# Kernel tuning notes

Measured on AMD Instinct MI355X. Metric: run time of the kernel, lower is better.

The kernel has to match this reference:

```python
import jax, jax.numpy as jnp
import numpy as np

EMBED = 1024

def setup_inputs() -> dict:
    key = jax.random.key(0)
    ks = jax.random.split(key, 7)
    s = 1.0 / np.sqrt(EMBED)
    x = jax.random.normal(ks[0], (8, 2048, EMBED), dtype=jnp.float32)
    Wq = jax.random.normal(ks[1], (EMBED, EMBED), dtype=jnp.float32) * s
    bq = jax.random.normal(ks[2], (EMBED,), dtype=jnp.float32) * s
    Wk = jax.random.normal(ks[3], (EMBED, EMBED), dtype=jnp.float32) * s
    bk = jax.random.normal(ks[4], (EMBED,), dtype=jnp.float32) * s
    Wv = jax.random.normal(ks[5], (EMBED, EMBED), dtype=jnp.float32) * s
    bv = jax.random.normal(ks[6], (EMBED,), dtype=jnp.float32) * s
    return {"x": x, "Wq": Wq, "bq": bq, "Wk": Wk, "bk": bk, "Wv": Wv, "bv": bv}

def reference(x, Wq, bq, Wk, bk, Wv, bv):
    # Linear layers: y = x @ W^T + b (torch convention)
    Q = jnp.einsum('bse,fe->bsf', x, Wq) + bq
    K = jnp.einsum('bse,fe->bsf', x, Wk) + bk
    V = jnp.einsum('bse,fe->bsf', x, Wv) + bv
    scale = 1.0 / jnp.sqrt(jnp.asarray(x.shape[-1], x.dtype))
    scores = jnp.einsum('bqe,bke->bqk', Q, K) * scale  # [B, S, S]
    weights = jax.nn.softmax(scores, axis=-1)
    # dropout is identity in eval mode (deterministic reference)
    return jnp.einsum('bqk,bke->bqe', weights, V)
```

## Files before the change

kernel.cpp:

```cpp
#include <hip/hip_runtime.h>

typedef __bf16 bf16x8 __attribute__((ext_vector_type(8)));
typedef float f32x4 __attribute__((ext_vector_type(4)));

__device__ __forceinline__ unsigned short f2bf(float f) {
  unsigned int u = __builtin_bit_cast(unsigned int, f);
  u += 0x7fffu + ((u >> 16) & 1u);
  return (unsigned short)(u >> 16);
}

__device__ __forceinline__ void async16(const void* g, void* l) {
  __builtin_amdgcn_global_load_lds(
      (const __attribute__((address_space(1))) unsigned int*)g,
      (__attribute__((address_space(3))) unsigned int*)l, 16, 0, 0);
}

#define MFMA(a, b, c) __builtin_amdgcn_mfma_f32_16x16x32_bf16((a), (b), (c), 0, 0, 0)

__global__ __launch_bounds__(256) void pack_bf16(const float* __restrict__ src,
                                                 unsigned short* __restrict__ dst,
                                                 long n) {
  long i = ((long)blockIdx.x * blockDim.x + threadIdx.x) * 4;
  long stride = (long)gridDim.x * blockDim.x * 4;
  for (; i < n; i += stride) {
    float4 v = *(const float4*)(src + i);
    ushort4 o;
    o.x = f2bf(v.x); o.y = f2bf(v.y); o.z = f2bf(v.z); o.w = f2bf(v.w);
    *(ushort4*)(dst + i) = o;
  }
}

__global__ __launch_bounds__(256) void pack_w3(const float* __restrict__ s0,
                                               const float* __restrict__ s1,
                                               const float* __restrict__ s2,
                                               unsigned short* __restrict__ dst) {
  const float* s = (blockIdx.y == 0) ? s0 : (blockIdx.y == 1) ? s1 : s2;
  long i = ((long)blockIdx.x * 256 + threadIdx.x) * 4;
  float4 v = *(const float4*)(s + i);
  ushort4 o;
  o.x = f2bf(v.x); o.y = f2bf(v.y); o.z = f2bf(v.z); o.w = f2bf(v.w);
  *(ushort4*)(dst + (long)blockIdx.y * 1048576 + i) = o;
}

template <int EPI>
__global__ __launch_bounds__(512, 1) void gemm256(
    const unsigned short* __restrict__ A, long sAz,
    const unsigned short* __restrict__ B, long sBz,
    int lda, int ldb, int nt,
    float* __restrict__ Cf, long sCz, int ldc, float scale,
    unsigned short* __restrict__ Cq, long sQz, int ldq,
    const float* __restrict__ bq, const float* __restrict__ bk,
    const float* __restrict__ bv, float* __restrict__ psum) {
  extern __shared__ __align__(16) char smem[];
  const int tid = threadIdx.x;
  const int l = tid & 63;
  const int w = tid >> 6;
  const int wm = w >> 2, wn = w & 3;
  int bm = blockIdx.x;
  if ((gridDim.x & 7) == 0) {
    int cpx = gridDim.x >> 3;
    bm = (bm & 7) * cpx + (bm >> 3);
  }
  const int bn = blockIdx.y, bz = blockIdx.z;
  const unsigned short* Ab = A + (long)bz * sAz + (long)bm * 256 * lda;
  const unsigned short* Bb = B + (long)bz * sBz + (long)bn * 256 * ldb;

  const int r0 = tid >> 3;
  const int sch = (tid & 7) ^ (r0 & 7);
  const int l15 = l & 15;
  const int kof = (l >> 4) << 3;

  const int aslot = wm * 16384;
  const int bslot = 32768 + (wn >> 1) * 16384;
  const int brow0 = (wn & 1) * 64;

  const int amask = (l15 & 7) << 4;
  const int acore0 = (aslot + l15 * 128 + kof * 2) ^ amask;
  const int acore1 = (aslot + l15 * 128 + 64 + kof * 2) ^ amask;
  const int bcore0 = (bslot + (brow0 + l15) * 128 + kof * 2) ^ amask;
  const int bcore1 = (bslot + (brow0 + l15) * 128 + 64 + kof * 2) ^ amask;

  const unsigned short* pa0 = Ab + (long)r0 * lda + sch * 8;
  const unsigned short* pa1 = pa0 + (long)64 * lda;
  const unsigned short* pa2 = pa0 + (long)128 * lda;
  const unsigned short* pa3 = pa0 + (long)192 * lda;
  const unsigned short* pb0 = Bb + (long)r0 * ldb + sch * 8;
  const unsigned short* pb1 = pb0 + (long)64 * ldb;
  const unsigned short* pb2 = pb0 + (long)128 * ldb;
  const unsigned short* pb3 = pb0 + (long)192 * ldb;

  char* sdst = smem + (tid << 4);

  f32x4 acc[8][4] = {};
  bf16x8 bfr[4][2];
  bf16x8 c00, c01, c10, c11;
  bf16x8 n00, n01, n10, n11;

#define LDA_F(dst, bb, fr, ks) \
  dst = *(const bf16x8*)(smem + (((ks) ? acore1 : acore0) + (fr)*2048 + (bb)));
#define LDB_F(dst, bb, fc, ks) \
  dst = *(const bf16x8*)(smem + (((ks) ? bcore1 : bcore0) + (fc)*2048 + (bb)));

  async16(pb0, sdst + 32768);         async16(pb1, sdst + 40960);
  async16(pb2, sdst + 49152);         async16(pb3, sdst + 57344);
  async16(pa0, sdst + 0);             async16(pa1, sdst + 8192);
  async16(pa2, sdst + 16384);         async16(pa3, sdst + 24576);
  async16(pb0 + 64, sdst + 98304);    async16(pb1 + 64, sdst + 106496);
  async16(pb2 + 64, sdst + 114688);   async16(pb3 + 64, sdst + 122880);
  asm volatile("s_waitcnt vmcnt(4)" ::: "memory");
  __builtin_amdgcn_s_barrier();
  pa0 += 64; pa1 += 64; pa2 += 64; pa3 += 64;
  pb0 += 128; pb1 += 128; pb2 += 128; pb3 += 128;

  LDA_F(c00, 0, 0, 0); LDA_F(c01, 0, 0, 1);
  LDA_F(c10, 0, 1, 0); LDA_F(c11, 0, 1, 1);

  for (int t = 0; t < nt; ++t) {
    const int buf = (t & 1) << 16;
    const int nbuf = buf ^ 65536;

#pragma unroll
    for (int fc = 0; fc < 4; ++fc) {
      LDB_F(bfr[fc][0], buf, fc, 0);
      LDB_F(bfr[fc][1], buf, fc, 1);
    }
    LDA_F(n00, buf, 2, 0); LDA_F(n01, buf, 2, 1);
    LDA_F(n10, buf, 3, 0); LDA_F(n11, buf, 3, 1);
    async16(pa0, sdst + nbuf);
    async16(pa1, sdst + nbuf + 8192);
    __builtin_amdgcn_s_setprio(1);
#pragma unroll
    for (int fc = 0; fc < 4; ++fc) {
      acc[0][fc] = MFMA(c00, bfr[fc][0], acc[0][fc]);
      acc[0][fc] = MFMA(c01, bfr[fc][1], acc[0][fc]);
      acc[1][fc] = MFMA(c10, bfr[fc][0], acc[1][fc]);
      acc[1][fc] = MFMA(c11, bfr[fc][1], acc[1][fc]);
    }
    __builtin_amdgcn_s_setprio(0);

    LDA_F(c00, buf, 4, 0); LDA_F(c01, buf, 4, 1);
    LDA_F(c10, buf, 5, 0); LDA_F(c11, buf, 5, 1);
    async16(pa2, sdst + nbuf + 16384);
    async16(pa3, sdst + nbuf + 24576);
    __builtin_amdgcn_s_setprio(1);
#pragma unroll
    for (int fc = 0; fc < 4; ++fc) {
      acc[2][fc] = MFMA(n00, bfr[fc][0], acc[2][fc]);
      acc[2][fc] = MFMA(n01, bfr[fc][1], acc[2][fc]);
      acc[3][fc] = MFMA(n10, bfr[fc][0], acc[3][fc]);
      acc[3][fc] = MFMA(n11, bfr[fc][1], acc[3][fc]);
    }
    __builtin_amdgcn_s_setprio(0);
    __builtin_amdgcn_s_barrier();

    LDA_F(n00, buf, 6, 0); LDA_F(n01, buf, 6, 1);
    LDA_F(n10, buf, 7, 0); LDA_F(n11, buf, 7, 1);
    async16(pb0, sdst + buf + 32768);
    async16(pb1, sdst + buf + 40960);
    __builtin_amdgcn_s_setprio(1);
#pragma unroll
    for (int fc = 0; fc < 4; ++fc) {
      acc[4][fc] = MFMA(c00, bfr[fc][0], acc[4][fc]);
      acc[4][fc] = MFMA(c01, bfr[fc][1], acc[4][fc]);
      acc[5][fc] = MFMA(c10, bfr[fc][0], acc[5][fc]);
      acc[5][fc] = MFMA(c11, bfr[fc][1], acc[5][fc]);
    }
    __builtin_amdgcn_s_setprio(0);

    async16(pb2, sdst + buf + 49152);
    async16(pb3, sdst + buf + 57344);
    __builtin_amdgcn_s_setprio(1);
#pragma unroll
    for (int fc = 0; fc < 4; ++fc) {
      acc[6][fc] = MFMA(n00, bfr[fc][0], acc[6][fc]);
      acc[6][fc] = MFMA(n01, bfr[fc][1], acc[6][fc]);
      acc[7][fc] = MFMA(n10, bfr[fc][0], acc[7][fc]);
      acc[7][fc] = MFMA(n11, bfr[fc][1], acc[7][fc]);
    }
    __builtin_amdgcn_s_setprio(0);
    asm volatile("s_waitcnt vmcnt(4)" ::: "memory");
    __builtin_amdgcn_s_barrier();

    LDA_F(c00, nbuf, 0, 0); LDA_F(c01, nbuf, 0, 1);
    LDA_F(c10, nbuf, 1, 0); LDA_F(c11, nbuf, 1, 1);

    if (t < nt - 2) { pa0 += 64; pa1 += 64; pa2 += 64; pa3 += 64; }
    if (t < nt - 3) { pb0 += 64; pb1 += 64; pb2 += 64; pb3 += 64; }
  }

  asm volatile("s_waitcnt vmcnt(0)" ::: "memory");
  __builtin_amdgcn_s_barrier();

  const int rl = (l >> 4) * 4;

  if constexpr (EPI == 0) {
    const int which = (bn * 256) >> 10;
    const int colbase = bn * 256 + wn * 64;
    const float* bias = (which == 0) ? bq : (which == 1) ? bk : bv;
    if (which < 2) {
#pragma unroll
      for (int fr = 0; fr < 8; ++fr)
#pragma unroll
        for (int fc = 0; fc < 4; ++fc) {
          int lc = fc * 16 + l15;
          float bv_ = bias[(colbase + lc) & 1023];
#pragma unroll
          for (int rr = 0; rr < 4; ++rr) {
            int lr = fr * 16 + rl + rr;
            int byte = w * 16384 + lr * 128 + lc * 2;
            byte ^= (lr & 7) << 4;
            *(unsigned short*)(smem + byte) = f2bf(acc[fr][fc][rr] + bv_);
          }
        }
      __syncthreads();
      const long brow = (long)bm * 256;
      const int cw0 = (bn * 256) & 1023;
#pragma unroll
      for (int it = 0; it < 16; ++it) {
        int f = it * 512 + tid;
        int r = f >> 5, ch = f & 31;
        int wv = (r >> 7) * 4 + (ch >> 3);
        int byte = wv * 16384 + (r & 127) * 128 + (ch & 7) * 16;
        byte ^= (r & 7) << 4;
        uint4 val = *(const uint4*)(smem + byte);
        unsigned short* d = Cq + (long)which * 16777216L +
                            (brow + r) * 1024 + cw0 + ch * 8;
        *(uint4*)d = val;
      }
    } else {
#pragma unroll
      for (int fr = 0; fr < 8; ++fr)
#pragma unroll
        for (int fc = 0; fc < 4; ++fc) {
          int lc = wn * 64 + fc * 16 + l15;
          float bv_ = bias[(colbase + fc * 16 + l15) & 1023];
#pragma unroll
          for (int rr = 0; rr < 4; ++rr) {
            int r = wm * 128 + fr * 16 + rl + rr;
            int byte = lc * 512 + r * 2;
            byte ^= (lc & 7) << 4;
            *(unsigned short*)(smem + byte) = f2bf(acc[fr][fc][rr] + bv_);
          }
        }
      __syncthreads();
      const long brow = (long)bm * 256;
      const long b = brow >> 11;
      const long s0 = brow & 2047;
      unsigned short* VT = Cq + 2L * 16777216;
#pragma unroll
      for (int it = 0; it < 16; ++it) {
        int f = it * 512 + tid;
        int c = f >> 5, ch = f & 31;
        int byte = (c * 512 + ch * 16) ^ ((c & 7) << 4);
        uint4 val = *(const uint4*)(smem + byte);
        int d = (bn * 256 - 2048) + c;
        unsigned short* dst = VT + b * 2097152 + (long)d * 2048 + s0 + ch * 8;
        *(uint4*)dst = val;
      }
    }
  } else if constexpr (EPI == 3) {
    float rs[4];
#pragma unroll
    for (int fr = 0; fr < 8; ++fr) {
      rs[0] = rs[1] = rs[2] = rs[3] = 0.0f;
#pragma unroll
      for (int fc = 0; fc < 4; ++fc) {
        int lc = fc * 16 + l15;
#pragma unroll
        for (int rr = 0; rr < 4; ++rr) {
          float e = __expf(acc[fr][fc][rr] * scale);
          rs[rr] += e;
          int lr = fr * 16 + rl + rr;
          int byte = w * 16384 + lr * 128 + lc * 2;
          byte ^= (lr & 7) << 4;
          *(unsigned short*)(smem + byte) = f2bf(e);
        }
      }
#pragma unroll
      for (int rr = 0; rr < 4; ++rr) {
        float v = rs[rr];
#pragma unroll
        for (int o = 1; o < 16; o <<= 1) v += __shfl_xor(v, o);
        if (l15 == 0) {
          int row = wm * 128 + fr * 16 + rl + rr;
          *(float*)(smem + 131072 + (wn * 256 + row) * 4) = v;
        }
      }
    }
    __syncthreads();
    const long brow = (long)bm * 256;
#pragma unroll
    for (int it = 0; it < 16; ++it) {
      int f = it * 512 + tid;
      int r = f >> 5, ch = f & 31;
      int wv = (r >> 7) * 4 + (ch >> 3);
      int byte = wv * 16384 + (r & 127) * 128 + (ch & 7) * 16;
      byte ^= (r & 7) << 4;
      uint4 val = *(const uint4*)(smem + byte);
      unsigned short* d = Cq + (long)bz * sQz + (brow + r) * ldq + bn * 256 + ch * 8;
      *(uint4*)d = val;
    }
    if (tid < 256) {
      float s4 = *(const float*)(smem + 131072 + tid * 4) +
                 *(const float*)(smem + 131072 + 1024 + tid * 4) +
                 *(const float*)(smem + 131072 + 2048 + tid * 4) +
                 *(const float*)(smem + 131072 + 3072 + tid * 4);
      psum[(((long)bz * 2048) + brow + tid) * 8 + bn] = s4;
    }
  } else {
    float* C = Cf + (long)bz * sCz;
    const long grbase = (long)bm * 256 + wm * 128;
    const int gcbase = bn * 256 + wn * 64;
#pragma unroll
    for (int fr = 0; fr < 8; ++fr)
#pragma unroll
      for (int rr = 0; rr < 4; ++rr) {
        long gr = grbase + fr * 16 + rl + rr;
        const float* pp = psum + (((long)bz * 2048) + gr) * 8;
        float4 s0 = *(const float4*)pp;
        float4 s1 = *(const float4*)(pp + 4);
        float inv = 1.0f / (s0.x + s0.y + s0.z + s0.w +
                            s1.x + s1.y + s1.z + s1.w);
#pragma unroll
        for (int fc = 0; fc < 4; ++fc)
          C[gr * ldc + gcbase + fc * 16 + l15] = acc[fr][fc][rr] * inv;
      }
  }
#undef LDA_F
#undef LDB_F
}

__global__ void sentinel_kernel(float* out, float v) { out[0] = v; }

extern "C" void kernel_launch(void* const* d_in, const int* in_sizes, int n_in,
                              void* d_out, int out_size, void* d_ws, size_t ws_size,
                              hipStream_t stream) {
  const float* x  = (const float*)d_in[0];
  const float* Wq = (const float*)d_in[1];
  const float* bq = (const float*)d_in[2];
  const float* Wk = (const float*)d_in[3];
  const float* bk = (const float*)d_in[4];
  const float* Wv = (const float*)d_in[5];
  const float* bv = (const float*)d_in[6];
  float* out = (float*)d_out;

  (void)hipFuncSetAttribute((const void*)gemm256<0>,
      hipFuncAttributeMaxDynamicSharedMemorySize, 135168);
  (void)hipFuncSetAttribute((const void*)gemm256<3>,
      hipFuncAttributeMaxDynamicSharedMemorySize, 135168);
  (void)hipFuncSetAttribute((const void*)gemm256<4>,
      hipFuncAttributeMaxDynamicSharedMemorySize, 135168);

  const size_t NEED_BIG2 = 208207872;
  const size_t NEED_SM2  = 140509184;
  if (ws_size < NEED_SM2) {
    sentinel_kernel<<<1, 1, 0, stream>>>(out, (float)ws_size);
    return;
  }
  const bool big = (ws_size >= NEED_BIG2);
  char* ws = (char*)d_ws;
  unsigned short* qkv = (unsigned short*)(ws);
  unsigned short* xb  = (unsigned short*)(ws + 100663296);
  unsigned short* wb  = (unsigned short*)(ws + 134217728);
  unsigned short* wt  = big ? (unsigned short*)(ws + 140509184)
                            : (unsigned short*)(ws + 100663296);
  float* psum = big ? (float*)(ws + 207618048) : (float*)(ws + 117440512);

  const float scale = 0.03125f;

  pack_bf16<<<dim3(4096), dim3(256), 0, stream>>>(x, xb, 16777216L);
  pack_w3<<<dim3(1024, 3), dim3(256), 0, stream>>>(Wq, Wk, Wv, wb);

  gemm256<0><<<dim3(64, 12, 1), dim3(512), 135168, stream>>>(
      xb, 0L, wb, 0L, 1024, 1024, 16,
      nullptr, 0L, 0, 1.0f, qkv, 0L, 1024, bq, bk, bv, nullptr);

  const int bpp = big ? 8 : 2;
  const int npasses = 8 / bpp;
  for (int p = 0; p < npasses; ++p) {
    long b0 = (long)p * bpp;
    long boff = b0 * 2048 * 1024;
    gemm256<3><<<dim3(8, 8, bpp), dim3(512), 135168, stream>>>(
        qkv + boff, 2048L * 1024, qkv + 16777216 + boff, 2048L * 1024,
        1024, 1024, 16,
        nullptr, 0L, 0, scale, wt, 2048L * 2048, 2048,
        nullptr, nullptr, nullptr, psum);

    gemm256<4><<<dim3(8, 4, bpp), dim3(512), 135168, stream>>>(
        wt, 2048L * 2048, qkv + 2L * 16777216 + b0 * 2097152, 2097152L,
        2048, 2048, 32,
        out + boff, 2048L * 1024, 1024, 1.0f, nullptr, 0L, 0,
        nullptr, nullptr, nullptr, psum);
  }
}
```

Measured before the change: 269.0 us.

## Shrink GEMM tiles to 128x256 with 32-wide K and triple-buffered B

Replaces the 256x256, K=64 GEMM tile with a 128x256 tile using K=32 steps, a new XOR swizzle, and a rotating triple buffer for B. LDS use drops to about 66KB and launch bounds allow more blocks per CU, so more warps can hide latency and the grid doubles for better CU coverage. The cost is less operand reuse per block, more global and L2 traffic, and more loop iterations with barriers. Epilogues are rewritten to stage output through LDS in two halves.

```diff
diff --git a/kernel.cpp b/kernel.cpp
--- a/kernel.cpp
+++ b/kernel.cpp
@@ -43,7 +43,7 @@
 }
 
 template <int EPI>
-__global__ __launch_bounds__(512, 1) void gemm256(
+__global__ __launch_bounds__(512, 4) void gemm128(
     const unsigned short* __restrict__ A, long sAz,
     const unsigned short* __restrict__ B, long sBz,
     int lda, int ldb, int nt,
@@ -62,130 +62,74 @@
     bm = (bm & 7) * cpx + (bm >> 3);
   }
   const int bn = blockIdx.y, bz = blockIdx.z;
-  const unsigned short* Ab = A + (long)bz * sAz + (long)bm * 256 * lda;
+  const unsigned short* Ab = A + (long)bz * sAz + (long)bm * 128 * lda;
   const unsigned short* Bb = B + (long)bz * sBz + (long)bn * 256 * ldb;
 
-  const int r0 = tid >> 3;
-  const int sch = (tid & 7) ^ (r0 & 7);
+  const int row0 = tid >> 2;
+  const int sch = (tid & 3) ^ (row0 & 3) ^ ((row0 >> 2) & 3);
   const int l15 = l & 15;
-  const int kof = (l >> 4) << 3;
-
-  const int aslot = wm * 16384;
-  const int bslot = 32768 + (wn >> 1) * 16384;
-  const int brow0 = (wn & 1) * 64;
-
-  const int amask = (l15 & 7) << 4;
-  const int acore0 = (aslot + l15 * 128 + kof * 2) ^ amask;
-  const int acore1 = (aslot + l15 * 128 + 64 + kof * 2) ^ amask;
-  const int bcore0 = (bslot + (brow0 + l15) * 128 + kof * 2) ^ amask;
-  const int bcore1 = (bslot + (brow0 + l15) * 128 + 64 + kof * 2) ^ amask;
-
-  const unsigned short* pa0 = Ab + (long)r0 * lda + sch * 8;
-  const unsigned short* pa1 = pa0 + (long)64 * lda;
-  const unsigned short* pa2 = pa0 + (long)128 * lda;
-  const unsigned short* pa3 = pa0 + (long)192 * lda;
-  const unsigned short* pb0 = Bb + (long)r0 * ldb + sch * 8;
-  const unsigned short* pb1 = pb0 + (long)64 * ldb;
-  const unsigned short* pb2 = pb0 + (long)128 * ldb;
-  const unsigned short* pb3 = pb0 + (long)192 * ldb;
-
-  char* sdst = smem + (tid << 4);
-
-  f32x4 acc[8][4] = {};
-  bf16x8 bfr[4][2];
-  bf16x8 c00, c01, c10, c11;
-  bf16x8 n00, n01, n10, n11;
-
-#define LDA_F(dst, bb, fr, ks) \
-  dst = *(const bf16x8*)(smem + (((ks) ? acore1 : acore0) + (fr)*2048 + (bb)));
-#define LDB_F(dst, bb, fc, ks) \
-  dst = *(const bf16x8*)(smem + (((ks) ? bcore1 : bcore0) + (fc)*2048 + (bb)));
-
-  async16(pb0, sdst + 32768);         async16(pb1, sdst + 40960);
-  async16(pb2, sdst + 49152);         async16(pb3, sdst + 57344);
-  async16(pa0, sdst + 0);             async16(pa1, sdst + 8192);
-  async16(pa2, sdst + 16384);         async16(pa3, sdst + 24576);
-  async16(pb0 + 64, sdst + 98304);    async16(pb1 + 64, sdst + 106496);
-  async16(pb2 + 64, sdst + 114688);   async16(pb3 + 64, sdst + 122880);
-  asm volatile("s_waitcnt vmcnt(4)" ::: "memory");
+  const int kc = l >> 4;
+
+  int aof[4], bof[4];
+#pragma unroll
+  for (int fr = 0; fr < 4; ++fr) {
+    int r = wm * 64 + fr * 16 + l15;
+    aof[fr] = r * 64 + ((kc ^ (r & 3) ^ ((r >> 2) & 3)) << 4);
+  }
+#pragma unroll
+  for (int fc = 0; fc < 4; ++fc) {
+    int r = wn * 64 + fc * 16 + l15;
+    bof[fc] = r * 64 + ((kc ^ (r & 3) ^ ((r >> 2) & 3)) << 4);
+  }
+
+  const unsigned short* pa  = Ab + (long)row0 * lda + sch * 8;
+  const unsigned short* pb0 = Bb + (long)row0 * ldb + sch * 8;
+  const unsigned short* pb1 = pb0 + (long)128 * ldb;
+  char* sd = smem + (tid << 4);
+
+  f32x4 acc[4][4] = {};
+  bf16x8 bf0, bf1, bf2, bf3, c0, c1, n0, n1;
+
+#define LDAF(dst, base, fr) dst = *(const bf16x8*)(smem + (base) + aof[fr]);
+#define LDBF(dst, base, fc) dst = *(const bf16x8*)(smem + (base) + bof[fc]);
+
+  async16(pb0, sd + 16384); async16(pb1, sd + 24576);
+  async16(pa, sd);
+  async16(pb0 + 32, sd + 32768); async16(pb1 + 32, sd + 40960);
+  asm volatile("s_waitcnt vmcnt(2)" ::: "memory");
   __builtin_amdgcn_s_barrier();
-  pa0 += 64; pa1 += 64; pa2 += 64; pa3 += 64;
-  pb0 += 128; pb1 += 128; pb2 += 128; pb3 += 128;
-
-  LDA_F(c00, 0, 0, 0); LDA_F(c01, 0, 0, 1);
-  LDA_F(c10, 0, 1, 0); LDA_F(c11, 0, 1, 1);
+  pa += 32; pb0 += 64; pb1 += 64;
+  int bR = 16384, bN = 32768, bS = 49152;
+  LDAF(c0, 0, 0); LDAF(c1, 0, 1);
 
   for (int t = 0; t < nt; ++t) {
-    const int buf = (t & 1) << 16;
-    const int nbuf = buf ^ 65536;
-
-#pragma unroll
-    for (int fc = 0; fc < 4; ++fc) {
-      LDB_F(bfr[fc][0], buf, fc, 0);
-      LDB_F(bfr[fc][1], buf, fc, 1);
-    }
-    LDA_F(n00, buf, 2, 0); LDA_F(n01, buf, 2, 1);
-    LDA_F(n10, buf, 3, 0); LDA_F(n11, buf, 3, 1);
-    async16(pa0, sdst + nbuf);
-    async16(pa1, sdst + nbuf + 8192);
+    const int abuf = (t & 1) << 13;
+    const int anb = abuf ^ 8192;
+
+    LDBF(bf0, bR, 0); LDBF(bf1, bR, 1); LDBF(bf2, bR, 2); LDBF(bf3, bR, 3);
+    LDAF(n0, abuf, 2); LDAF(n1, abuf, 3);
+    async16(pa, sd + anb);
     __builtin_amdgcn_s_setprio(1);
-#pragma unroll
-    for (int fc = 0; fc < 4; ++fc) {
-      acc[0][fc] = MFMA(c00, bfr[fc][0], acc[0][fc]);
-      acc[0][fc] = MFMA(c01, bfr[fc][1], acc[0][fc]);
-      acc[1][fc] = MFMA(c10, bfr[fc][0], acc[1][fc]);
-      acc[1][fc] = MFMA(c11, bfr[fc][1], acc[1][fc]);
-    }
+    acc[0][0] = MFMA(c0, bf0, acc[0][0]); acc[0][1] = MFMA(c0, bf1, acc[0][1]);
+    acc[0][2] = MFMA(c0, bf2, acc[0][2]); acc[0][3] = MFMA(c0, bf3, acc[0][3]);
+    acc[1][0] = MFMA(c1, bf0, acc[1][0]); acc[1][1] = MFMA(c1, bf1, acc[1][1]);
+    acc[1][2] = MFMA(c1, bf2, acc[1][2]); acc[1][3] = MFMA(c1, bf3, acc[1][3]);
     __builtin_amdgcn_s_setprio(0);
 
-    LDA_F(c00, buf, 4, 0); LDA_F(c01, buf, 4, 1);
-    LDA_F(c10, buf, 5, 0); LDA_F(c11, buf, 5, 1);
-    async16(pa2, sdst + nbuf + 16384);
-    async16(pa3, sdst + nbuf + 24576);
+    async16(pb0, sd + bS); async16(pb1, sd + bS + 8192);
     __builtin_amdgcn_s_setprio(1);
-#pragma unroll
-    for (int fc = 0; fc < 4; ++fc) {
-      acc[2][fc] = MFMA(n00, bfr[fc][0], acc[2][fc]);
-      acc[2][fc] = MFMA(n01, bfr[fc][1], acc[2][fc]);
-      acc[3][fc] = MFMA(n10, bfr[fc][0], acc[3][fc]);
-      acc[3][fc] = MFMA(n11, bfr[fc][1], acc[3][fc]);
-    }
+    acc[2][0] = MFMA(n0, bf0, acc[2][0]); acc[2][1] = MFMA(n0, bf1, acc[2][1]);
+    acc[2][2] = MFMA(n0, bf2, acc[2][2]); acc[2][3] = MFMA(n0, bf3, acc[2][3]);
+    acc[3][0] = MFMA(n1, bf0, acc[3][0]); acc[3][1] = MFMA(n1, bf1, acc[3][1]);
+    acc[3][2] = MFMA(n1, bf2, acc[3][2]); acc[3][3] = MFMA(n1, bf3, acc[3][3]);
     __builtin_amdgcn_s_setprio(0);
+    asm volatile("s_waitcnt vmcnt(2)" ::: "memory");
     __builtin_amdgcn_s_barrier();
 
-    LDA_F(n00, buf, 6, 0); LDA_F(n01, buf, 6, 1);
-    LDA_F(n10, buf, 7, 0); LDA_F(n11, buf, 7, 1);
-    async16(pb0, sdst + buf + 32768);
-    async16(pb1, sdst + buf + 40960);
-    __builtin_amdgcn_s_setprio(1);
-#pragma unroll
-    for (int fc = 0; fc < 4; ++fc) {
-      acc[4][fc] = MFMA(c00, bfr[fc][0], acc[4][fc]);
-      acc[4][fc] = MFMA(c01, bfr[fc][1], acc[4][fc]);
-      acc[5][fc] = MFMA(c10, bfr[fc][0], acc[5][fc]);
-      acc[5][fc] = MFMA(c11, bfr[fc][1], acc[5][fc]);
-    }
-    __builtin_amdgcn_s_setprio(0);
-
-    async16(pb2, sdst + buf + 49152);
-    async16(pb3, sdst + buf + 57344);
-    __builtin_amdgcn_s_setprio(1);
-#pragma unroll
-    for (int fc = 0; fc < 4; ++fc) {
-      acc[6][fc] = MFMA(n00, bfr[fc][0], acc[6][fc]);
-      acc[6][fc] = MFMA(n01, bfr[fc][1], acc[6][fc]);
-      acc[7][fc] = MFMA(n10, bfr[fc][0], acc[7][fc]);
-      acc[7][fc] = MFMA(n11, bfr[fc][1], acc[7][fc]);
-    }
-    __builtin_amdgcn_s_setprio(0);
-    asm volatile("s_waitcnt vmcnt(4)" ::: "memory");
-    __builtin_amdgcn_s_barrier();
-
-    LDA_F(c00, nbuf, 0, 0); LDA_F(c01, nbuf, 0, 1);
-    LDA_F(c10, nbuf, 1, 0); LDA_F(c11, nbuf, 1, 1);
-
-    if (t < nt - 2) { pa0 += 64; pa1 += 64; pa2 += 64; pa3 += 64; }
-    if (t < nt - 3) { pb0 += 64; pb1 += 64; pb2 += 64; pb3 += 64; }
+    LDAF(c0, anb, 0); LDAF(c1, anb, 1);
+    int tmp = bR; bR = bN; bN = bS; bS = tmp;
+    if (t < nt - 2) pa += 32;
+    if (t < nt - 3) { pb0 += 32; pb1 += 32; }
   }
 
   asm volatile("s_waitcnt vmcnt(0)" ::: "memory");
@@ -195,124 +139,142 @@
 
   if constexpr (EPI == 0) {
     const int which = (bn * 256) >> 10;
-    const int colbase = bn * 256 + wn * 64;
     const float* bias = (which == 0) ? bq : (which == 1) ? bk : bv;
-    if (which < 2) {
-#pragma unroll
-      for (int fr = 0; fr < 8; ++fr)
-#pragma unroll
-        for (int fc = 0; fc < 4; ++fc) {
-          int lc = fc * 16 + l15;
-          float bv_ = bias[(colbase + lc) & 1023];
-#pragma unroll
-          for (int rr = 0; rr < 4; ++rr) {
-            int lr = fr * 16 + rl + rr;
-            int byte = w * 16384 + lr * 128 + lc * 2;
-            byte ^= (lr & 7) << 4;
-            *(unsigned short*)(smem + byte) = f2bf(acc[fr][fc][rr] + bv_);
-          }
-        }
+    const long brow = (long)bm * 128;
+#pragma unroll
+    for (int r = 0; r < 2; ++r) {
+      if ((wn >> 1) == r) {
+        if (which < 2) {
+#pragma unroll
+          for (int fr = 0; fr < 4; ++fr)
+#pragma unroll
+            for (int fc = 0; fc < 4; ++fc) {
+              int cc = (wn & 1) * 64 + fc * 16 + l15;
+              float bv_ = bias[(bn * 256 + r * 128 + cc) & 1023];
+#pragma unroll
+              for (int rr = 0; rr < 4; ++rr) {
+                int lr = wm * 64 + fr * 16 + rl + rr;
+                int byte = (lr * 256 + cc * 2) ^ (((lr >> 2) & 3) << 4);
+                *(unsigned short*)(smem + byte) = f2bf(acc[fr][fc][rr] + bv_);
+              }
+            }
+        } else {
+#pragma unroll
+          for (int fr = 0; fr < 4; ++fr)
+#pragma unroll
+            for (int fc = 0; fc < 4; ++fc) {
+              int cc = (wn & 1) * 64 + fc * 16 + l15;
+              float bv_ = bias[(bn * 256 + r * 128 + cc) & 1023];
+#pragma unroll
+              for (int rr = 0; rr < 4; ++rr) {
+                int srow = wm * 64 + fr * 16 + rl + rr;
+                int byte = (cc * 256 + srow * 2) ^
+                           ((((cc & 3) ^ ((cc >> 2) & 3))) << 4);
+                *(unsigned short*)(smem + byte) = f2bf(acc[fr][fc][rr] + bv_);
+              }
+            }
+        }
+      }
       __syncthreads();
-      const long brow = (long)bm * 256;
-      const int cw0 = (bn * 256) & 1023;
-#pragma unroll
-      for (int it = 0; it < 16; ++it) {
-        int f = it * 512 + tid;
-        int r = f >> 5, ch = f & 31;
-        int wv = (r >> 7) * 4 + (ch >> 3);
-        int byte = wv * 16384 + (r & 127) * 128 + (ch & 7) * 16;
-        byte ^= (r & 7) << 4;
-        uint4 val = *(const uint4*)(smem + byte);
-        unsigned short* d = Cq + (long)which * 16777216L +
-                            (brow + r) * 1024 + cw0 + ch * 8;
-        *(uint4*)d = val;
-      }
-    } else {
-#pragma unroll
-      for (int fr = 0; fr < 8; ++fr)
-#pragma unroll
-        for (int fc = 0; fc < 4; ++fc) {
-          int lc = wn * 64 + fc * 16 + l15;
-          float bv_ = bias[(colbase + fc * 16 + l15) & 1023];
-#pragma unroll
-          for (int rr = 0; rr < 4; ++rr) {
-            int r = wm * 128 + fr * 16 + rl + rr;
-            int byte = lc * 512 + r * 2;
-            byte ^= (lc & 7) << 4;
-            *(unsigned short*)(smem + byte) = f2bf(acc[fr][fc][rr] + bv_);
-          }
-        }
+      if (which < 2) {
+#pragma unroll
+        for (int it = 0; it < 4; ++it) {
+          int f = it * 512 + tid;
+          int row = f >> 4, ch = f & 15;
+          int byte = (row * 256 + ch * 16) ^ (((row >> 2) & 3) << 4);
+          uint4 val = *(const uint4*)(smem + byte);
+          unsigned short* d = Cq + (long)which * 16777216L +
+                              (brow + row) * 1024 +
+                              ((bn * 256 + r * 128) & 1023) + ch * 8;
+          *(uint4*)d = val;
+        }
+      } else {
+        const long b = brow >> 11;
+        const long s0 = brow & 2047;
+        unsigned short* VT = Cq + 2L * 16777216;
+#pragma unroll
+        for (int it = 0; it < 2; ++it) {
+          int f = it * 512 + tid;
+          int c = f >> 3, sch2 = f & 7;
+          int swz = (c & 3) ^ ((c >> 2) & 3);
+          int base = c * 256;
+          uint4 v0 = *(const uint4*)(smem + base + (((2 * sch2) ^ swz) << 4));
+          uint4 v1 = *(const uint4*)(smem + base + (((2 * sch2 + 1) ^ swz) << 4));
+          int d = bn * 256 - 2048 + r * 128 + c;
+          unsigned short* dst = VT + b * 2097152 + (long)d * 2048 + s0 + sch2 * 16;
+          *(uint4*)dst = v0;
+          *(uint4*)(dst + 8) = v1;
+        }
+      }
       __syncthreads();
-      const long brow = (long)bm * 256;
-      const long b = brow >> 11;
-      const long s0 = brow & 2047;
-      unsigned short* VT = Cq + 2L * 16777216;
-#pragma unroll
-      for (int it = 0; it < 16; ++it) {
-        int f = it * 512 + tid;
-        int c = f >> 5, ch = f & 31;
-        int byte = (c * 512 + ch * 16) ^ ((c & 7) << 4);
-        uint4 val = *(const uint4*)(smem + byte);
-        int d = (bn * 256 - 2048) + c;
-        unsigned short* dst = VT + b * 2097152 + (long)d * 2048 + s0 + ch * 8;
-        *(uint4*)dst = val;
-      }
     }
   } else if constexpr (EPI == 3) {
-    float rs[4];
-#pragma unroll
-    for (int fr = 0; fr < 8; ++fr) {
-      rs[0] = rs[1] = rs[2] = rs[3] = 0.0f;
-#pragma unroll
-      for (int fc = 0; fc < 4; ++fc) {
-        int lc = fc * 16 + l15;
+#pragma unroll
+    for (int fr = 0; fr < 4; ++fr) {
+      float rs[4] = {0.f, 0.f, 0.f, 0.f};
+#pragma unroll
+      for (int fc = 0; fc < 4; ++fc)
 #pragma unroll
         for (int rr = 0; rr < 4; ++rr) {
           float e = __expf(acc[fr][fc][rr] * scale);
+          acc[fr][fc][rr] = e;
           rs[rr] += e;
-          int lr = fr * 16 + rl + rr;
-          int byte = w * 16384 + lr * 128 + lc * 2;
-          byte ^= (lr & 7) << 4;
-          *(unsigned short*)(smem + byte) = f2bf(e);
-        }
-      }
+        }
 #pragma unroll
       for (int rr = 0; rr < 4; ++rr) {
         float v = rs[rr];
 #pragma unroll
         for (int o = 1; o < 16; o <<= 1) v += __shfl_xor(v, o);
         if (l15 == 0) {
-          int row = wm * 128 + fr * 16 + rl + rr;
-          *(float*)(smem + 131072 + (wn * 256 + row) * 4) = v;
+          int row = wm * 64 + fr * 16 + rl + rr;
+          *(float*)(smem + 65536 + (wn * 128 + row) * 4) = v;
         }
       }
     }
     __syncthreads();
-    const long brow = (long)bm * 256;
-#pragma unroll
-    for (int it = 0; it < 16; ++it) {
-      int f = it * 512 + tid;
-      int r = f >> 5, ch = f & 31;
-      int wv = (r >> 7) * 4 + (ch >> 3);
-      int byte = wv * 16384 + (r & 127) * 128 + (ch & 7) * 16;
-      byte ^= (r & 7) << 4;
-      uint4 val = *(const uint4*)(smem + byte);
-      unsigned short* d = Cq + (long)bz * sQz + (brow + r) * ldq + bn * 256 + ch * 8;
-      *(uint4*)d = val;
+    const long brow = (long)bm * 128;
+    if (tid < 128) {
+      float s4 = *(const float*)(smem + 65536 + tid * 4) +
+                 *(const float*)(smem + 65536 + 512 + tid * 4) +
+                 *(const float*)(smem + 65536 + 1024 + tid * 4) +
+                 *(const float*)(smem + 65536 + 1536 + tid * 4);
+      psum[(((long)bz * 2048) + brow + tid) * 8 + bn] = s4;
     }
-    if (tid < 256) {
-      float s4 = *(const float*)(smem + 131072 + tid * 4) +
-                 *(const float*)(smem + 131072 + 1024 + tid * 4) +
-                 *(const float*)(smem + 131072 + 2048 + tid * 4) +
-                 *(const float*)(smem + 131072 + 3072 + tid * 4);
-      psum[(((long)bz * 2048) + brow + tid) * 8 + bn] = s4;
+#pragma unroll
+    for (int r = 0; r < 2; ++r) {
+      if ((wn >> 1) == r) {
+#pragma unroll
+        for (int fr = 0; fr < 4; ++fr)
+#pragma unroll
+          for (int fc = 0; fc < 4; ++fc) {
+            int cc = (wn & 1) * 64 + fc * 16 + l15;
+#pragma unroll
+            for (int rr = 0; rr < 4; ++rr) {
+              int lr = wm * 64 + fr * 16 + rl + rr;
+              int byte = (lr * 256 + cc * 2) ^ (((lr >> 2) & 3) << 4);
+              *(unsigned short*)(smem + byte) = f2bf(acc[fr][fc][rr]);
+            }
+          }
+      }
+      __syncthreads();
+#pragma unroll
+      for (int it = 0; it < 4; ++it) {
+        int f = it * 512 + tid;
+        int row = f >> 4, ch = f & 15;
+        int byte = (row * 256 + ch * 16) ^ (((row >> 2) & 3) << 4);
+        uint4 val = *(const uint4*)(smem + byte);
+        unsigned short* d = Cq + (long)bz * sQz + (brow + row) * ldq +
+                            bn * 256 + r * 128 + ch * 8;
+        *(uint4*)d = val;
+      }
+      __syncthreads();
     }
   } else {
     float* C = Cf + (long)bz * sCz;
-    const long grbase = (long)bm * 256 + wm * 128;
+    const long grbase = (long)bm * 128 + wm * 64;
     const int gcbase = bn * 256 + wn * 64;
 #pragma unroll
-    for (int fr = 0; fr < 8; ++fr)
+    for (int fr = 0; fr < 4; ++fr)
 #pragma unroll
       for (int rr = 0; rr < 4; ++rr) {
         long gr = grbase + fr * 16 + rl + rr;
@@ -326,8 +288,8 @@
           C[gr * ldc + gcbase + fc * 16 + l15] = acc[fr][fc][rr] * inv;
       }
   }
-#undef LDA_F
-#undef LDB_F
+#undef LDAF
+#undef LDBF
 }
 
 __global__ void sentinel_kernel(float* out, float v) { out[0] = v; }
@@ -344,12 +306,12 @@
   const float* bv = (const float*)d_in[6];
   float* out = (float*)d_out;
 
-  (void)hipFuncSetAttribute((const void*)gemm256<0>,
-      hipFuncAttributeMaxDynamicSharedMemorySize, 135168);
-  (void)hipFuncSetAttribute((const void*)gemm256<3>,
-      hipFuncAttributeMaxDynamicSharedMemorySize, 135168);
-  (void)hipFuncSetAttribute((const void*)gemm256<4>,
-      hipFuncAttributeMaxDynamicSharedMemorySize, 135168);
+  (void)hipFuncSetAttribute((const void*)gemm128<0>,
+      hipFuncAttributeMaxDynamicSharedMemorySize, 67584);
+  (void)hipFuncSetAttribute((const void*)gemm128<3>,
+      hipFuncAttributeMaxDynamicSharedMemorySize, 67584);
+  (void)hipFuncSetAttribute((const void*)gemm128<4>,
+      hipFuncAttributeMaxDynamicSharedMemorySize, 67584);
 
   const size_t NEED_BIG2 = 208207872;
   const size_t NEED_SM2  = 140509184;
@@ -371,8 +333,8 @@
   pack_bf16<<<dim3(4096), dim3(256), 0, stream>>>(x, xb, 16777216L);
   pack_w3<<<dim3(1024, 3), dim3(256), 0, stream>>>(Wq, Wk, Wv, wb);
 
-  gemm256<0><<<dim3(64, 12, 1), dim3(512), 135168, stream>>>(
-      xb, 0L, wb, 0L, 1024, 1024, 16,
+  gemm128<0><<<dim3(128, 12, 1), dim3(512), 67584, stream>>>(
+      xb, 0L, wb, 0L, 1024, 1024, 32,
       nullptr, 0L, 0, 1.0f, qkv, 0L, 1024, bq, bk, bv, nullptr);
 
   const int bpp = big ? 8 : 2;
@@ -380,15 +342,15 @@
   for (int p = 0; p < npasses; ++p) {
     long b0 = (long)p * bpp;
     long boff = b0 * 2048 * 1024;
-    gemm256<3><<<dim3(8, 8, bpp), dim3(512), 135168, stream>>>(
+    gemm128<3><<<dim3(16, 8, bpp), dim3(512), 67584, stream>>>(
         qkv + boff, 2048L * 1024, qkv + 16777216 + boff, 2048L * 1024,
-        1024, 1024, 16,
+        1024, 1024, 32,
         nullptr, 0L, 0, scale, wt, 2048L * 2048, 2048,
         nullptr, nullptr, nullptr, psum);
 
-    gemm256<4><<<dim3(8, 4, bpp), dim3(512), 135168, stream>>>(
+    gemm128<4><<<dim3(16, 4, bpp), dim3(512), 67584, stream>>>(
         wt, 2048L * 2048, qkv + 2L * 16777216 + b0 * 2097152, 2097152L,
-        2048, 2048, 32,
+        2048, 2048, 64,
         out + boff, 2048L * 1024, 1024, 1.0f, nullptr, 0L, 0,
         nullptr, nullptr, nullptr, psum);
   }
```

Result: slower. 301.5 us (+12.1%).

## Triple-buffer B tiles in LDS and drop the mid-iteration barrier

Applied to the files above, without the earlier changes.

The B operand gets three rotating LDS slots (current, next, staging) while A keeps its two. New B tiles are written into the staging slot, so the barrier that used to protect reuse of the current B buffer in the middle of each iteration is removed. B fragments for the next iteration are now loaded into registers right after the end-of-iteration barrier. Dynamic shared memory grows to 160 KB per block. That fills the whole LDS and keeps B fragments live across the barrier, which may raise register pressure.

```diff
diff --git a/kernel.cpp b/kernel.cpp
--- a/kernel.cpp
+++ b/kernel.cpp
@@ -71,14 +71,14 @@
   const int kof = (l >> 4) << 3;
 
   const int aslot = wm * 16384;
-  const int bslot = 32768 + (wn >> 1) * 16384;
+  const int bslotRel = (wn >> 1) * 16384;
   const int brow0 = (wn & 1) * 64;
 
   const int amask = (l15 & 7) << 4;
   const int acore0 = (aslot + l15 * 128 + kof * 2) ^ amask;
   const int acore1 = (aslot + l15 * 128 + 64 + kof * 2) ^ amask;
-  const int bcore0 = (bslot + (brow0 + l15) * 128 + kof * 2) ^ amask;
-  const int bcore1 = (bslot + (brow0 + l15) * 128 + 64 + kof * 2) ^ amask;
+  const int bcore0 = (bslotRel + (brow0 + l15) * 128 + kof * 2) ^ amask;
+  const int bcore1 = (bslotRel + (brow0 + l15) * 128 + 64 + kof * 2) ^ amask;
 
   const unsigned short* pa0 = Ab + (long)r0 * lda + sch * 8;
   const unsigned short* pa1 = pa0 + (long)64 * lda;
@@ -101,8 +101,8 @@
 #define LDB_F(dst, bb, fc, ks) \
   dst = *(const bf16x8*)(smem + (((ks) ? bcore1 : bcore0) + (fc)*2048 + (bb)));
 
-  async16(pb0, sdst + 32768);         async16(pb1, sdst + 40960);
-  async16(pb2, sdst + 49152);         async16(pb3, sdst + 57344);
+  async16(pb0, sdst + 65536);         async16(pb1, sdst + 73728);
+  async16(pb2, sdst + 81920);         async16(pb3, sdst + 90112);
   async16(pa0, sdst + 0);             async16(pa1, sdst + 8192);
   async16(pa2, sdst + 16384);         async16(pa3, sdst + 24576);
   async16(pb0 + 64, sdst + 98304);    async16(pb1 + 64, sdst + 106496);
@@ -112,22 +112,24 @@
   pa0 += 64; pa1 += 64; pa2 += 64; pa3 += 64;
   pb0 += 128; pb1 += 128; pb2 += 128; pb3 += 128;
 
+  int bCur = 65536, bNxt = 98304, bStg = 131072;
+
   LDA_F(c00, 0, 0, 0); LDA_F(c01, 0, 0, 1);
   LDA_F(c10, 0, 1, 0); LDA_F(c11, 0, 1, 1);
+#pragma unroll
+  for (int fc = 0; fc < 4; ++fc) {
+    LDB_F(bfr[fc][0], bCur, fc, 0);
+    LDB_F(bfr[fc][1], bCur, fc, 1);
+  }
 
   for (int t = 0; t < nt; ++t) {
-    const int buf = (t & 1) << 16;
-    const int nbuf = buf ^ 65536;
-
-#pragma unroll
-    for (int fc = 0; fc < 4; ++fc) {
-      LDB_F(bfr[fc][0], buf, fc, 0);
-      LDB_F(bfr[fc][1], buf, fc, 1);
-    }
-    LDA_F(n00, buf, 2, 0); LDA_F(n01, buf, 2, 1);
-    LDA_F(n10, buf, 3, 0); LDA_F(n11, buf, 3, 1);
-    async16(pa0, sdst + nbuf);
-    async16(pa1, sdst + nbuf + 8192);
+    const int abuf = (t & 1) << 15;
+    const int anb = abuf ^ 32768;
+
+    LDA_F(n00, abuf, 2, 0); LDA_F(n01, abuf, 2, 1);
+    LDA_F(n10, abuf, 3, 0); LDA_F(n11, abuf, 3, 1);
+    async16(pa0, sdst + anb);
+    async16(pa1, sdst + anb + 8192);
     __builtin_amdgcn_s_setprio(1);
 #pragma unroll
     for (int fc = 0; fc < 4; ++fc) {
@@ -138,10 +140,10 @@
     }
     __builtin_amdgcn_s_setprio(0);
 
-    LDA_F(c00, buf, 4, 0); LDA_F(c01, buf, 4, 1);
-    LDA_F(c10, buf, 5, 0); LDA_F(c11, buf, 5, 1);
-    async16(pa2, sdst + nbuf + 16384);
-    async16(pa3, sdst + nbuf + 24576);
+    LDA_F(c00, abuf, 4, 0); LDA_F(c01, abuf, 4, 1);
+    LDA_F(c10, abuf, 5, 0); LDA_F(c11, abuf, 5, 1);
+    async16(pa2, sdst + anb + 16384);
+    async16(pa3, sdst + anb + 24576);
     __builtin_amdgcn_s_setprio(1);
 #pragma unroll
     for (int fc = 0; fc < 4; ++fc) {
@@ -151,12 +153,11 @@
       acc[3][fc] = MFMA(n11, bfr[fc][1], acc[3][fc]);
     }
     __builtin_amdgcn_s_setprio(0);
-    __builtin_amdgcn_s_barrier();
-
-    LDA_F(n00, buf, 6, 0); LDA_F(n01, buf, 6, 1);
-    LDA_F(n10, buf, 7, 0); LDA_F(n11, buf, 7, 1);
-    async16(pb0, sdst + buf + 32768);
-    async16(pb1, sdst + buf + 40960);
+
+    LDA_F(n00, abuf, 6, 0); LDA_F(n01, abuf, 6, 1);
+    LDA_F(n10, abuf, 7, 0); LDA_F(n11, abuf, 7, 1);
+    async16(pb0, sdst + bStg);
+    async16(pb1, sdst + bStg + 8192);
     __builtin_amdgcn_s_setprio(1);
 #pragma unroll
     for (int fc = 0; fc < 4; ++fc) {
@@ -167,8 +168,8 @@
     }
     __builtin_amdgcn_s_setprio(0);
 
-    async16(pb2, sdst + buf + 49152);
-    async16(pb3, sdst + buf + 57344);
+    async16(pb2, sdst + bStg + 16384);
+    async16(pb3, sdst + bStg + 24576);
     __builtin_amdgcn_s_setprio(1);
 #pragma unroll
     for (int fc = 0; fc < 4; ++fc) {
@@ -180,10 +181,14 @@
     __builtin_amdgcn_s_setprio(0);
     asm volatile("s_waitcnt vmcnt(4)" ::: "memory");
     __builtin_amdgcn_s_barrier();
-
-    LDA_F(c00, nbuf, 0, 0); LDA_F(c01, nbuf, 0, 1);
-    LDA_F(c10, nbuf, 1, 0); LDA_F(c11, nbuf, 1, 1);
-
+    LDA_F(c00, anb, 0, 0); LDA_F(c01, anb, 0, 1);
+    LDA_F(c10, anb, 1, 0); LDA_F(c11, anb, 1, 1);
+#pragma unroll
+    for (int fc = 0; fc < 4; ++fc) {
+      LDB_F(bfr[fc][0], bNxt, fc, 0);
+      LDB_F(bfr[fc][1], bNxt, fc, 1);
+    }
+    int tmp = bCur; bCur = bNxt; bNxt = bStg; bStg = tmp;
     if (t < nt - 2) { pa0 += 64; pa1 += 64; pa2 += 64; pa3 += 64; }
     if (t < nt - 3) { pb0 += 64; pb1 += 64; pb2 += 64; pb3 += 64; }
   }
@@ -345,11 +350,11 @@
   float* out = (float*)d_out;
 
   (void)hipFuncSetAttribute((const void*)gemm256<0>,
-      hipFuncAttributeMaxDynamicSharedMemorySize, 135168);
+      hipFuncAttributeMaxDynamicSharedMemorySize, 163840);
   (void)hipFuncSetAttribute((const void*)gemm256<3>,
-      hipFuncAttributeMaxDynamicSharedMemorySize, 135168);
+      hipFuncAttributeMaxDynamicSharedMemorySize, 163840);
   (void)hipFuncSetAttribute((const void*)gemm256<4>,
-      hipFuncAttributeMaxDynamicSharedMemorySize, 135168);
+      hipFuncAttributeMaxDynamicSharedMemorySize, 163840);
 
   const size_t NEED_BIG2 = 208207872;
   const size_t NEED_SM2  = 140509184;
@@ -371,7 +376,7 @@
   pack_bf16<<<dim3(4096), dim3(256), 0, stream>>>(x, xb, 16777216L);
   pack_w3<<<dim3(1024, 3), dim3(256), 0, stream>>>(Wq, Wk, Wv, wb);
 
-  gemm256<0><<<dim3(64, 12, 1), dim3(512), 135168, stream>>>(
+  gemm256<0><<<dim3(64, 12, 1), dim3(512), 163840, stream>>>(
       xb, 0L, wb, 0L, 1024, 1024, 16,
       nullptr, 0L, 0, 1.0f, qkv, 0L, 1024, bq, bk, bv, nullptr);
 
@@ -380,13 +385,13 @@
   for (int p = 0; p < npasses; ++p) {
     long b0 = (long)p * bpp;
     long boff = b0 * 2048 * 1024;
-    gemm256<3><<<dim3(8, 8, bpp), dim3(512), 135168, stream>>>(
+    gemm256<3><<<dim3(8, 8, bpp), dim3(512), 163840, stream>>>(
         qkv + boff, 2048L * 1024, qkv + 16777216 + boff, 2048L * 1024,
         1024, 1024, 16,
         nullptr, 0L, 0, scale, wt, 2048L * 2048, 2048,
         nullptr, nullptr, nullptr, psum);
 
-    gemm256<4><<<dim3(8, 4, bpp), dim3(512), 135168, stream>>>(
+    gemm256<4><<<dim3(8, 4, bpp), dim3(512), 163840, stream>>>(
         wt, 2048L * 2048, qkv + 2L * 16777216 + b0 * 2097152, 2097152L,
         2048, 2048, 32,
         out + boff, 2048L * 1024, 1024, 1.0f, nullptr, 0L, 0,
```

Result: no change. 270.3 us (+0.5%).
